# Optimization experiments

Hardware: AMD Instinct MI355X
Metric: run time of the kernel (lower is better)

## Reference

```python
import jax, jax.numpy as jnp
import numpy as np

B, S, D, H = 2, 2048, 1024, 16
HD = D // H  # 64
EPS = 1e-6


def setup_inputs() -> dict:
    key = jax.random.key(0)
    ks = jax.random.split(key, 12)
    s = 1.0 / np.sqrt(D)
    return {
        "query": jax.random.normal(ks[0], (B, S, D), jnp.float32),
        "key": jax.random.normal(ks[1], (B, S, D), jnp.float32),
        "value": jax.random.normal(ks[2], (B, S, D), jnp.float32),
        "mask": jax.random.randint(ks[3], (B, S, S), 0, 2) == 1,
        "Wq": jax.random.normal(ks[4], (D, D), jnp.float32) * s,
        "bq": jnp.zeros((D,), jnp.float32),
        "Wk": jax.random.normal(ks[5], (D, D), jnp.float32) * s,
        "bk": jnp.zeros((D,), jnp.float32),
        "Wv": jax.random.normal(ks[6], (D, D), jnp.float32) * s,
        "bv": jnp.zeros((D,), jnp.float32),
        "Wo": jax.random.normal(ks[7], (D, D), jnp.float32) * s,
        "bo": jnp.zeros((D,), jnp.float32),
        "gamma": jnp.ones((D,), jnp.float32),
        "beta": jnp.zeros((D,), jnp.float32),
    }


def reference(query, key, value, mask, Wq, bq, Wk, bk, Wv, bv, Wo, bo, gamma, beta):
    b, sq, _ = query.shape
    sk = key.shape[1]
    # QKV projections -> [b, h, s, hd]
    q = (query @ Wq + bq).reshape(b, sq, H, HD).transpose(0, 2, 1, 3)
    k = (key @ Wk + bk).reshape(b, sk, H, HD).transpose(0, 2, 1, 3)
    v = (value @ Wv + bv).reshape(b, sk, H, HD).transpose(0, 2, 1, 3)
    # scores [b, h, sq, sk]
    scores = jnp.einsum("bhqd,bhkd->bhqk", q, k) / jnp.sqrt(jnp.float32(HD))
    scores = jnp.where(mask[:, None, :, :], -jnp.inf, scores)
    attn = jax.nn.softmax(scores, axis=-1)  # dropout: eval mode (identity)
    out = jnp.einsum("bhqk,bhkd->bhqd", attn, v)
    out = out.transpose(0, 2, 1, 3).reshape(b, sq, H * HD)
    out = out @ Wo + bo
    # residual + LayerNorm with unbiased std and (std + eps) denominator (faithful to torch code)
    x = query + out
    mean = x.mean(-1, keepdims=True)
    std = jnp.std(x, axis=-1, keepdims=True, ddof=1)
    return gamma * (x - mean) / (std + EPS) + beta
```

## Files before the change

### kernel.cpp

```cpp
#include <hip/hip_runtime.h>


#define NB 2
#define SS 2048
#define DDIM 1024
#define NH 16
#define HDIM 64
#define MROWS (NB * SS)

typedef unsigned short u16;
typedef unsigned long long u64;
typedef unsigned int u32;
typedef short bf16x8 __attribute__((ext_vector_type(8)));
typedef float f32x4 __attribute__((ext_vector_type(4)));

typedef const __attribute__((address_space(1))) void GASV;
typedef __attribute__((address_space(3))) void LASV;

__device__ __forceinline__ float dev_exp2(float x) {
  float r;
  asm("v_exp_f32 %0, %1" : "=v"(r) : "v"(x));
  return r;
}

__device__ __forceinline__ u16 f2bf(float f) {
  unsigned u = __builtin_bit_cast(unsigned, f);
  u += 0x7FFFu + ((u >> 16) & 1u);
  return (u16)(u >> 16);
}

__device__ __forceinline__ u32 cvt_pk_bf16(float a, float b) {
  u32 d;
  asm("v_cvt_pk_bf16_f32 %0, %1, %2" : "=v"(d) : "v"(a), "v"(b));
  return d;
}

__global__ __launch_bounds__(256) void cvt_bf16_3(const float* __restrict__ q,
                                                  const float* __restrict__ k,
                                                  const float* __restrict__ v,
                                                  u16* __restrict__ out) {
  const float* in = (blockIdx.y == 0) ? q : (blockIdx.y == 1) ? k : v;
  size_t i = ((size_t)blockIdx.x * 256 + threadIdx.x) * 4;
  float4 val = *(const float4*)(in + i);
  uint2 o;
  u16* po = (u16*)&o;
  po[0] = f2bf(val.x); po[1] = f2bf(val.y); po[2] = f2bf(val.z); po[3] = f2bf(val.w);
  *(uint2*)(out + (size_t)blockIdx.y * MROWS * DDIM + i) = o;
}

__global__ __launch_bounds__(256) void cvt_mask_bits(const int* __restrict__ in,
                                                     u64* __restrict__ out) {
  size_t w = ((size_t)blockIdx.x * 256 + threadIdx.x) >> 6;
  int lane = threadIdx.x & 63;
  int v = in[w * 64 + lane];
  u64 bits = __ballot(v != 0);
  if (lane == 0) out[w] = bits;
}

__global__ __launch_bounds__(256) void transpose_cvt_w4(const float* __restrict__ W0,
                                                        const float* __restrict__ W1,
                                                        const float* __restrict__ W2,
                                                        const float* __restrict__ W3,
                                                        u16* __restrict__ WTbase) {
  __shared__ u16 t[64][65];
  const int z = blockIdx.z;
  const float* W = (z == 0) ? W0 : (z == 1) ? W1 : (z == 2) ? W2 : W3;
  u16* WT = WTbase + (size_t)z * DDIM * DDIM;
  const int k0 = blockIdx.x * 64, n0 = blockIdx.y * 64;
  const int tid = threadIdx.x;
  const int r = tid >> 4;
  const int c4 = (tid & 15) * 4;
#pragma unroll
  for (int it = 0; it < 4; ++it) {
    int k = r + it * 16;
    float4 v = *(const float4*)&W[(size_t)(k0 + k) * DDIM + n0 + c4];
    t[c4 + 0][k] = f2bf(v.x);
    t[c4 + 1][k] = f2bf(v.y);
    t[c4 + 2][k] = f2bf(v.z);
    t[c4 + 3][k] = f2bf(v.w);
  }
  __syncthreads();
#pragma unroll
  for (int it = 0; it < 4; ++it) {
    int n = r + it * 16;
    uint2 o;
    u16* po = (u16*)&o;
#pragma unroll
    for (int j = 0; j < 4; ++j) po[j] = t[n][c4 + j];
    *(uint2*)&WT[(size_t)(n0 + n) * DDIM + k0 + c4] = o;
  }
}

template <int MODE>
__global__ __launch_bounds__(256) void gemm_bt(const u16* __restrict__ Abase,
                                               const u16* __restrict__ BT,
                                               const float* __restrict__ b0,
                                               const float* __restrict__ b1,
                                               const float* __restrict__ b2,
                                               const float* __restrict__ resid,
                                               void* __restrict__ C,
                                               void* __restrict__ Cv) {
  __shared__ __align__(16) u16 SMEM[2][2][128][64];
  u16(&Al)[2][128][64] = SMEM[0];
  u16(&Bl)[2][128][64] = SMEM[1];
  const int tid = threadIdx.x;
  const int wid = tid >> 6, lane = tid & 63;
  const int wm = (wid >> 1) * 64, wn = (wid & 1) * 64;
  const int NCOL = (MODE == 0) ? 24 : 8;
  const int lin = blockIdx.y * 32 + blockIdx.x;
  const int xcd = lin & 7, idx = lin >> 3;
  const int rowA0 = (xcd * 4 + idx / NCOL) * 128;
  const int colB0 = (idx % NCOL) * 128;
  const int sel = (MODE == 0) ? (colB0 >> 10) : 0;
  const u16* Ag = Abase + (size_t)sel * ((size_t)MROWS * DDIM) + (size_t)rowA0 * DDIM;
  const u16* Bg = BT + (size_t)colB0 * DDIM;
  f32x4 acc[4][4] = {};
  const int rl = lane >> 3;
  const int ce = (lane & 7) * 8;

#define G_STAGE(buf, kt)                                                       \
  do {                                                                         \
    _Pragma("unroll") for (int c = 0; c < 4; ++c) {                            \
      int rt = wid * 32 + c * 8;                                               \
      __builtin_amdgcn_global_load_lds(                                        \
          (GASV*)(Ag + (size_t)(rt + rl) * DDIM + (kt) + ce),                  \
          (LASV*)((char*)&Al[buf][0][0] + rt * 128), 16, 0, 0);                \
      __builtin_amdgcn_global_load_lds(                                        \
          (GASV*)(Bg + (size_t)(rt + rl) * DDIM + (kt) + ce),                  \
          (LASV*)((char*)&Bl[buf][0][0] + rt * 128), 16, 0, 0);                \
    }                                                                          \
  } while (0)

  G_STAGE(0, 0);
  __syncthreads();
  for (int t = 0; t < 16; ++t) {
    const int cur = t & 1;
    if (t < 15) G_STAGE(cur ^ 1, (t + 1) * 64);
#pragma unroll
    for (int kk = 0; kk < 64; kk += 32) {
      bf16x8 af[4], bfr[4];
#pragma unroll
      for (int i = 0; i < 4; ++i)
        af[i] = *(const bf16x8*)&Al[cur][wm + i * 16 + (lane & 15)][kk + (lane >> 4) * 8];
#pragma unroll
      for (int j = 0; j < 4; ++j)
        bfr[j] = *(const bf16x8*)&Bl[cur][wn + j * 16 + (lane & 15)][kk + (lane >> 4) * 8];
#pragma unroll
      for (int i = 0; i < 4; ++i)
#pragma unroll
        for (int j = 0; j < 4; ++j)
          acc[i][j] = __builtin_amdgcn_mfma_f32_16x16x32_bf16(af[i], bfr[j], acc[i][j], 0, 0, 0);
    }
    __syncthreads();
  }
#undef G_STAGE

  const int cb = lane & 15, hi = lane >> 4;
  if (MODE == 0) {
    if (sel == 2) {
      u16(*T)[136] = (u16(*)[136]) & SMEM[0][0][0][0];
      const int dcol0 = colB0 & 1023;
#pragma unroll
      for (int j = 0; j < 4; ++j) {
        int dl = wn + j * 16 + cb;
        float bv = b2[dcol0 + dl];
#pragma unroll
        for (int i = 0; i < 4; ++i) {
          int sl = wm + i * 16 + hi * 4;
          uint2 o;
          o.x = cvt_pk_bf16(acc[i][j][0] + bv, acc[i][j][1] + bv);
          o.y = cvt_pk_bf16(acc[i][j][2] + bv, acc[i][j][3] + bv);
          *(uint2*)&T[dl][sl] = o;
        }
      }
      __syncthreads();
      const int bb = rowA0 >> 11, s0 = rowA0 & (SS - 1);
#pragma unroll
      for (int it = 0; it < 8; ++it) {
        int chunk = it * 256 + tid;
        int dl = chunk >> 4;
        int sc = (chunk & 15) * 8;
        int dg = dcol0 + dl;
        *(bf16x8*)&((u16*)Cv)[((size_t)(bb * NH + (dg >> 6)) * HDIM + (dg & 63)) * SS +
                              s0 + sc] = *(const bf16x8*)&T[dl][sc];
      }
    } else {
      const float* bp = (sel == 0) ? b0 : b1;
      const float scale = (sel == 0) ? 0.125f * 1.44269504088896340736f : 1.0f;
      u16* dst = (u16*)C + (size_t)sel * ((size_t)MROWS * DDIM);
      const int colw0 = (colB0 & 1023) + wn;
#pragma unroll
      for (int i = 0; i < 4; ++i)
#pragma unroll
        for (int j = 0; j < 4; ++j) {
          int colw = colw0 + j * 16 + cb;
          float bv = bp[colw];
#pragma unroll
          for (int r = 0; r < 4; ++r) {
            int row = rowA0 + wm + i * 16 + hi * 4 + r;
            dst[(size_t)row * DDIM + colw] = f2bf((acc[i][j][r] + bv) * scale);
          }
        }
    }
  } else {
#pragma unroll
    for (int i = 0; i < 4; ++i)
#pragma unroll
      for (int j = 0; j < 4; ++j) {
        int col = colB0 + wn + j * 16 + cb;
        float bv = b0[col];
#pragma unroll
        for (int r = 0; r < 4; ++r) {
          int row = rowA0 + wm + i * 16 + hi * 4 + r;
          size_t off = (size_t)row * DDIM + col;
          ((float*)C)[off] = acc[i][j][r] + bv + resid[off];
        }
      }
  }
}

__global__ __launch_bounds__(512, 4) void attn_fwd(const u16* __restrict__ Qp,
                                                   const u16* __restrict__ Kp,
                                                   const u16* __restrict__ VpT,
                                                   const u64* __restrict__ Mbits,
                                                   u16* __restrict__ O) {
  __shared__ __align__(16) u16 Kl[3][64][64];
  __shared__ __align__(16) u16 Vl[3][64][64];
  __shared__ __align__(16) u16 Pl[8][16][64];
  const int tid = threadIdx.x, wid = tid >> 6, lane = tid & 63;
  const int bid = blockIdx.x;
  const int bh = (bid & 7) * 4 + ((bid >> 3) & 3);
  const int q0 = (bid >> 5) * 128;
  const int b = bh >> 4, h = bh & 15;
  const int hi = lane >> 4, cbase = lane & 15, lx = lane & 7;

  bf16x8 qf[2];
  {
    const u16* qb = Qp + (size_t)(b * SS + q0 + wid * 16 + cbase) * DDIM + h * 64 + hi * 8;
    qf[0] = *(const bf16x8*)qb;
    qf[1] = *(const bf16x8*)(qb + 32);
  }
  const bf16x8 ONES8 = {(short)0x3F80, (short)0x3F80, (short)0x3F80, (short)0x3F80,
                        (short)0x3F80, (short)0x3F80, (short)0x3F80, (short)0x3F80};
  f32x4 l_acc = (f32x4){0.f, 0.f, 0.f, 0.f};
  f32x4 accO[4];
#pragma unroll
  for (int f = 0; f < 4; ++f) accO[f] = (f32x4){0.f, 0.f, 0.f, 0.f};

  const u16* Kgb = Kp + (size_t)b * SS * DDIM + h * 64;
  const u16* Vgb = VpT + (size_t)bh * 64 * SS;
  const u64* Mb = Mbits + (size_t)(b * SS + q0 + wid * 16 + cbase) * (SS / 64);
  const int rl = lane >> 3;
  const int ceS = ((lane & 7) ^ rl) * 8;

  int fo[4][2];
#pragma unroll
  for (int f = 0; f < 4; ++f)
#pragma unroll
    for (int ks = 0; ks < 2; ++ks)
      fo[f][ks] = (f * 16 + cbase) * 64 + (((ks * 4 + hi) ^ lx) << 3);
  int pw[4];
#pragma unroll
  for (int f = 0; f < 4; ++f)
    pw[f] = cbase * 64 + (((f * 2 + (hi >> 1)) ^ lx) << 3) + ((hi & 1) << 2);
  u16* KlF = &Kl[0][0][0];
  u16* VlF = &Vl[0][0][0];
  u16* Plw = &Pl[wid][0][0];

#define STAGE_KV(BUF, kv)                                                      \
  do {                                                                         \
    int rt = wid * 8;                                                          \
    __builtin_amdgcn_global_load_lds(                                          \
        (GASV*)(Kgb + (size_t)((kv) + rt + rl) * DDIM + ceS),                  \
        (LASV*)((char*)KlF + (BUF) * 8192 + rt * 128), 16, 0, 0);              \
    __builtin_amdgcn_global_load_lds(                                          \
        (GASV*)(Vgb + (size_t)(rt + rl) * SS + (kv) + ceS),                    \
        (LASV*)((char*)VlF + (BUF) * 8192 + rt * 128), 16, 0, 0);              \
  } while (0)

#define WAITVM(N) asm volatile("s_waitcnt vmcnt(" #N ")" ::: "memory")

#define ATTN_ITER(T, BUF, DO_STAGE, VM)                                        \
  do {                                                                         \
    WAITVM(VM);                                                                \
    __builtin_amdgcn_s_barrier();                                              \
    u64 mrow = Mb[T];                                                          \
    if (DO_STAGE) STAGE_KV(((BUF) + 2) % 3, ((T) + 2) * 64);                   \
    f32x4 sc[4];                                                               \
    __builtin_amdgcn_s_setprio(1);                                             \
    _Pragma("unroll") for (int fn = 0; fn < 4; ++fn) {                         \
      f32x4 c = (f32x4){0.f, 0.f, 0.f, 0.f};                                   \
      _Pragma("unroll") for (int ks = 0; ks < 2; ++ks) {                       \
        bf16x8 kf = *(const bf16x8*)(KlF + (BUF) * 4096 + fo[fn][ks]);         \
        c = __builtin_amdgcn_mfma_f32_16x16x32_bf16(kf, qf[ks], c, 0, 0, 0);   \
      }                                                                        \
      sc[fn] = c;                                                              \
    }                                                                          \
    __builtin_amdgcn_s_setprio(0);                                             \
             \
    u64 mh = mrow >> (hi * 4);                                                 \
    u32 mlo = (u32)mh, mhi2 = (u32)(mh >> 32);                                 \
    _Pragma("unroll") for (int fn = 0; fn < 4; ++fn) {                         \
      u32 b4 = ((fn < 2) ? mlo : mhi2) >> ((fn & 1) * 16);                     \
      _Pragma("unroll") for (int j = 0; j < 4; ++j) {                          \
        float bf_ = (float)((b4 >> j) & 1u);                                   \
        sc[fn][j] = dev_exp2(fmaf(bf_, -512.f, sc[fn][j]));                    \
      }                                                                        \
    }                                                                          \
    _Pragma("unroll") for (int fn = 0; fn < 4; ++fn) {                         \
      uint2 wpair;                                                             \
      wpair.x = cvt_pk_bf16(sc[fn][0], sc[fn][1]);                             \
      wpair.y = cvt_pk_bf16(sc[fn][2], sc[fn][3]);                             \
      *(uint2*)(Plw + pw[fn]) = wpair;                                         \
    }                                                                          \
    bf16x8 pf0 = *(const bf16x8*)(Plw + fo[0][0]);                             \
    bf16x8 pf1 = *(const bf16x8*)(Plw + fo[0][1]);                             \
    __builtin_amdgcn_s_setprio(1);                                             \
    l_acc = __builtin_amdgcn_mfma_f32_16x16x32_bf16(pf0, ONES8, l_acc, 0, 0, 0); \
    l_acc = __builtin_amdgcn_mfma_f32_16x16x32_bf16(pf1, ONES8, l_acc, 0, 0, 0); \
    _Pragma("unroll") for (int nd = 0; nd < 4; ++nd) {                         \
      bf16x8 v0 = *(const bf16x8*)(VlF + (BUF) * 4096 + fo[nd][0]);            \
      bf16x8 v1 = *(const bf16x8*)(VlF + (BUF) * 4096 + fo[nd][1]);            \
      accO[nd] = __builtin_amdgcn_mfma_f32_16x16x32_bf16(pf0, v0, accO[nd], 0, 0, 0); \
      accO[nd] = __builtin_amdgcn_mfma_f32_16x16x32_bf16(pf1, v1, accO[nd], 0, 0, 0); \
    }                                                                          \
    __builtin_amdgcn_s_setprio(0);                                             \
  } while (0)

  STAGE_KV(0, 0);
  STAGE_KV(1, 64);
  for (int t3 = 0; t3 < 30; t3 += 3) {
    ATTN_ITER(t3 + 0, 0, true, 2);
    ATTN_ITER(t3 + 1, 1, true, 2);
    ATTN_ITER(t3 + 2, 2, true, 2);
  }
  ATTN_ITER(30, 0, false, 2);
  ATTN_ITER(31, 1, false, 0);
#undef ATTN_ITER
#undef WAITVM
#undef STAGE_KV

#pragma unroll
  for (int nd = 0; nd < 4; ++nd)
#pragma unroll
    for (int j = 0; j < 4; ++j) {
      int row = q0 + wid * 16 + hi * 4 + j;
      int col = h * 64 + nd * 16 + cbase;
      O[(size_t)(b * SS + row) * DDIM + col] = f2bf(accO[nd][j] / l_acc[j]);
    }
}

__global__ __launch_bounds__(256) void ln_res(const float* __restrict__ xin,
                                              const float* __restrict__ gamma,
                                              const float* __restrict__ beta,
                                              float* __restrict__ out) {
  const int tid = threadIdx.x, wid = tid >> 6, lane = tid & 63;
  const int row = blockIdx.x * 4 + wid;
  const float* xr = xin + (size_t)row * DDIM;
  float4 x[4];
  float s = 0.f;
#pragma unroll
  for (int i = 0; i < 4; ++i) {
    x[i] = *(const float4*)(xr + lane * 4 + i * 256);
    s += (x[i].x + x[i].y) + (x[i].z + x[i].w);
  }
#pragma unroll
  for (int off = 32; off >= 1; off >>= 1) s += __shfl_xor(s, off, 64);
  float mean = s * (1.0f / DDIM);
  float ss = 0.f;
#pragma unroll
  for (int i = 0; i < 4; ++i) {
    x[i].x -= mean; x[i].y -= mean; x[i].z -= mean; x[i].w -= mean;
    ss += (x[i].x * x[i].x + x[i].y * x[i].y) + (x[i].z * x[i].z + x[i].w * x[i].w);
  }
#pragma unroll
  for (int off = 32; off >= 1; off >>= 1) ss += __shfl_xor(ss, off, 64);
  float var = ss * (1.0f / (DDIM - 1));
  float rden = 1.0f / (sqrtf(var) + 1e-6f);
  float* orow = out + (size_t)row * DDIM;
#pragma unroll
  for (int i = 0; i < 4; ++i) {
    float4 g = *(const float4*)(gamma + lane * 4 + i * 256);
    float4 be = *(const float4*)(beta + lane * 4 + i * 256);
    float4 o;
    o.x = g.x * x[i].x * rden + be.x;
    o.y = g.y * x[i].y * rden + be.y;
    o.z = g.z * x[i].z * rden + be.z;
    o.w = g.w * x[i].w * rden + be.w;
    *(float4*)(orow + lane * 4 + i * 256) = o;
  }
}

extern "C" void kernel_launch(void* const* d_in, const int* in_sizes, int n_in,
                              void* d_out, int out_size, void* d_ws, size_t ws_size,
                              hipStream_t stream) {
  const float* query = (const float*)d_in[0];
  const float* key = (const float*)d_in[1];
  const float* value = (const float*)d_in[2];
  const int* mask = (const int*)d_in[3];
  const float* Wq = (const float*)d_in[4];
  const float* bq = (const float*)d_in[5];
  const float* Wk = (const float*)d_in[6];
  const float* bk = (const float*)d_in[7];
  const float* Wv = (const float*)d_in[8];
  const float* bv = (const float*)d_in[9];
  const float* Wo = (const float*)d_in[10];
  const float* bo = (const float*)d_in[11];
  const float* gamma = (const float*)d_in[12];
  const float* beta = (const float*)d_in[13];
  float* out = (float*)d_out;
  char* ws = (char*)d_ws;
  const size_t MB = 1ull << 20;
  u16* qkvb = (u16*)(ws + 0 * MB);
  u16* WT = (u16*)(ws + 24 * MB);
  u16* WoT = (u16*)(ws + 30 * MB);
  u16* Qp = (u16*)(ws + 32 * MB);
  u16* Kp = (u16*)(ws + 40 * MB);
  u16* VpT = (u16*)(ws + 48 * MB);
  u16* attnb = (u16*)(ws + 56 * MB);
  u64* maskbits = (u64*)(ws + 0 * MB);
  float* proj = (float*)(ws + 8 * MB);

  cvt_bf16_3<<<dim3(MROWS * DDIM / 1024, 3), 256, 0, stream>>>(query, key, value, qkvb);
  transpose_cvt_w4<<<dim3(16, 16, 4), 256, 0, stream>>>(Wq, Wk, Wv, Wo, WT);
  gemm_bt<0><<<dim3(32, 24), 256, 0, stream>>>(qkvb, WT, bq, bk, bv, nullptr, Qp, VpT);
  cvt_mask_bits<<<(NB * SS * SS) / 256, 256, 0, stream>>>(mask, maskbits);
  attn_fwd<<<512, 512, 0, stream>>>(Qp, Kp, VpT, maskbits, attnb);
  gemm_bt<1><<<dim3(32, 8), 256, 0, stream>>>(attnb, WoT, bo, nullptr, nullptr,
                                              query, proj, nullptr);
  ln_res<<<MROWS / 4, 256, 0, stream>>>(proj, gamma, beta, out);
}
```

Measured before the change: 153.2 us.

## Fuse fp32-to-bf16 input conversion into QKV GEMM and merge weight/mask prep kernels

The QKV GEMM now loads fp32 query/key/value straight into registers, converts them to bf16 and writes them to LDS, which removes the separate conversion kernel and its 24MB round trip. The weight transpose and mask bit-packing kernels are merged into a single launch. The cost is that the A-tile path no longer uses the async global-to-LDS load. It now needs extra registers and a register-staged write after the MFMA loop, and it reads twice as many bytes per A tile.

New measurement: 171.3 us. 1.12x slower.

```diff
diff --git a/kernel.cpp b/kernel.cpp
--- a/kernel.cpp
+++ b/kernel.cpp
@@ -35,64 +35,55 @@
   return d;
 }
 
-__global__ __launch_bounds__(256) void cvt_bf16_3(const float* __restrict__ q,
-                                                  const float* __restrict__ k,
-                                                  const float* __restrict__ v,
-                                                  u16* __restrict__ out) {
-  const float* in = (blockIdx.y == 0) ? q : (blockIdx.y == 1) ? k : v;
-  size_t i = ((size_t)blockIdx.x * 256 + threadIdx.x) * 4;
-  float4 val = *(const float4*)(in + i);
-  uint2 o;
-  u16* po = (u16*)&o;
-  po[0] = f2bf(val.x); po[1] = f2bf(val.y); po[2] = f2bf(val.z); po[3] = f2bf(val.w);
-  *(uint2*)(out + (size_t)blockIdx.y * MROWS * DDIM + i) = o;
-}
-
-__global__ __launch_bounds__(256) void cvt_mask_bits(const int* __restrict__ in,
-                                                     u64* __restrict__ out) {
-  size_t w = ((size_t)blockIdx.x * 256 + threadIdx.x) >> 6;
-  int lane = threadIdx.x & 63;
-  int v = in[w * 64 + lane];
-  u64 bits = __ballot(v != 0);
-  if (lane == 0) out[w] = bits;
-}
-
-__global__ __launch_bounds__(256) void transpose_cvt_w4(const float* __restrict__ W0,
-                                                        const float* __restrict__ W1,
-                                                        const float* __restrict__ W2,
-                                                        const float* __restrict__ W3,
-                                                        u16* __restrict__ WTbase) {
-  __shared__ u16 t[64][65];
-  const int z = blockIdx.z;
-  const float* W = (z == 0) ? W0 : (z == 1) ? W1 : (z == 2) ? W2 : W3;
-  u16* WT = WTbase + (size_t)z * DDIM * DDIM;
-  const int k0 = blockIdx.x * 64, n0 = blockIdx.y * 64;
-  const int tid = threadIdx.x;
-  const int r = tid >> 4;
-  const int c4 = (tid & 15) * 4;
-#pragma unroll
-  for (int it = 0; it < 4; ++it) {
-    int k = r + it * 16;
-    float4 v = *(const float4*)&W[(size_t)(k0 + k) * DDIM + n0 + c4];
-    t[c4 + 0][k] = f2bf(v.x);
-    t[c4 + 1][k] = f2bf(v.y);
-    t[c4 + 2][k] = f2bf(v.z);
-    t[c4 + 3][k] = f2bf(v.w);
-  }
-  __syncthreads();
-#pragma unroll
-  for (int it = 0; it < 4; ++it) {
-    int n = r + it * 16;
-    uint2 o;
-    u16* po = (u16*)&o;
-#pragma unroll
-    for (int j = 0; j < 4; ++j) po[j] = t[n][c4 + j];
-    *(uint2*)&WT[(size_t)(n0 + n) * DDIM + k0 + c4] = o;
+__global__ __launch_bounds__(256) void prep_wm(const float* __restrict__ W0,
+                                               const float* __restrict__ W1,
+                                               const float* __restrict__ W2,
+                                               const float* __restrict__ W3,
+                                               u16* __restrict__ WTbase,
+                                               const int* __restrict__ maskin,
+                                               u64* __restrict__ mbits) {
+  const int bid = blockIdx.x, tid = threadIdx.x;
+  if (bid < 1024) {
+    __shared__ u16 t[64][65];
+    const int z = bid >> 8;
+    const float* W = (z == 0) ? W0 : (z == 1) ? W1 : (z == 2) ? W2 : W3;
+    u16* WT = WTbase + (size_t)z * DDIM * DDIM;
+    const int k0 = ((bid >> 4) & 15) * 64, n0 = (bid & 15) * 64;
+    const int r = tid >> 4;
+    const int c4 = (tid & 15) * 4;
+#pragma unroll
+    for (int it = 0; it < 4; ++it) {
+      int k = r + it * 16;
+      float4 v = *(const float4*)&W[(size_t)(k0 + k) * DDIM + n0 + c4];
+      t[c4 + 0][k] = f2bf(v.x);
+      t[c4 + 1][k] = f2bf(v.y);
+      t[c4 + 2][k] = f2bf(v.z);
+      t[c4 + 3][k] = f2bf(v.w);
+    }
+    __syncthreads();
+#pragma unroll
+    for (int it = 0; it < 4; ++it) {
+      int n = r + it * 16;
+      uint2 o;
+      u16* po = (u16*)&o;
+#pragma unroll
+      for (int j = 0; j < 4; ++j) po[j] = t[n][c4 + j];
+      *(uint2*)&WT[(size_t)(n0 + n) * DDIM + k0 + c4] = o;
+    }
+  } else {
+    size_t w = ((size_t)(bid - 1024) * 256 + tid) >> 6;
+    int lane = tid & 63;
+    int v = maskin[w * 64 + lane];
+    u64 bits = __ballot(v != 0);
+    if (lane == 0) mbits[w] = bits;
   }
 }
 
 template <int MODE>
-__global__ __launch_bounds__(256) void gemm_bt(const u16* __restrict__ Abase,
+__global__ __launch_bounds__(256) void gemm_bt(const float* __restrict__ Af0,
+                                               const float* __restrict__ Af1,
+                                               const float* __restrict__ Af2,
+                                               const u16* __restrict__ Abf,
                                                const u16* __restrict__ BT,
                                                const float* __restrict__ b0,
                                                const float* __restrict__ b1,
@@ -112,30 +103,79 @@
   const int rowA0 = (xcd * 4 + idx / NCOL) * 128;
   const int colB0 = (idx % NCOL) * 128;
   const int sel = (MODE == 0) ? (colB0 >> 10) : 0;
-  const u16* Ag = Abase + (size_t)sel * ((size_t)MROWS * DDIM) + (size_t)rowA0 * DDIM;
+  const float* Af = nullptr;
+  const u16* Ag = nullptr;
+  if (MODE == 0) {
+    Af = ((sel == 0) ? Af0 : (sel == 1) ? Af1 : Af2) + (size_t)rowA0 * DDIM;
+  } else {
+    Ag = Abf + (size_t)rowA0 * DDIM;
+  }
   const u16* Bg = BT + (size_t)colB0 * DDIM;
   f32x4 acc[4][4] = {};
   const int rl = lane >> 3;
   const int ce = (lane & 7) * 8;
 
-#define G_STAGE(buf, kt)                                                       \
+  float4 pa0[4], pa1[4];
+
+#define A_LOADF(kt)                                                            \
+  do {                                                                         \
+    _Pragma("unroll") for (int c = 0; c < 4; ++c) {                            \
+      int row = wid * 32 + c * 8 + rl;                                         \
+      pa0[c] = *(const float4*)(Af + (size_t)row * DDIM + (kt) + ce);          \
+      pa1[c] = *(const float4*)(Af + (size_t)row * DDIM + (kt) + ce + 4);      \
+    }                                                                          \
+  } while (0)
+
+#define A_WRITEF(buf)                                                          \
+  do {                                                                         \
+    _Pragma("unroll") for (int c = 0; c < 4; ++c) {                            \
+      int row = wid * 32 + c * 8 + rl;                                         \
+      bf16x8 w;                                                                \
+      u32* pw32 = (u32*)&w;                                                    \
+      pw32[0] = cvt_pk_bf16(pa0[c].x, pa0[c].y);                               \
+      pw32[1] = cvt_pk_bf16(pa0[c].z, pa0[c].w);                               \
+      pw32[2] = cvt_pk_bf16(pa1[c].x, pa1[c].y);                               \
+      pw32[3] = cvt_pk_bf16(pa1[c].z, pa1[c].w);                               \
+      *(bf16x8*)&Al[buf][row][ce] = w;                                         \
+    }                                                                          \
+  } while (0)
+
+#define A_GLOAD(buf, kt)                                                       \
   do {                                                                         \
     _Pragma("unroll") for (int c = 0; c < 4; ++c) {                            \
       int rt = wid * 32 + c * 8;                                               \
       __builtin_amdgcn_global_load_lds(                                        \
           (GASV*)(Ag + (size_t)(rt + rl) * DDIM + (kt) + ce),                  \
           (LASV*)((char*)&Al[buf][0][0] + rt * 128), 16, 0, 0);                \
+    }                                                                          \
+  } while (0)
+
+#define B_STAGE(buf, kt)                                                       \
+  do {                                                                         \
+    _Pragma("unroll") for (int c = 0; c < 4; ++c) {                            \
+      int rt = wid * 32 + c * 8;                                               \
       __builtin_amdgcn_global_load_lds(                                        \
           (GASV*)(Bg + (size_t)(rt + rl) * DDIM + (kt) + ce),                  \
           (LASV*)((char*)&Bl[buf][0][0] + rt * 128), 16, 0, 0);                \
     }                                                                          \
   } while (0)
 
-  G_STAGE(0, 0);
+  if (MODE == 0) {
+    A_LOADF(0);
+    B_STAGE(0, 0);
+    A_WRITEF(0);
+  } else {
+    A_GLOAD(0, 0);
+    B_STAGE(0, 0);
+  }
   __syncthreads();
   for (int t = 0; t < 16; ++t) {
     const int cur = t & 1;
-    if (t < 15) G_STAGE(cur ^ 1, (t + 1) * 64);
+    if (t < 15) {
+      if (MODE == 0) A_LOADF((t + 1) * 64);
+      else A_GLOAD(cur ^ 1, (t + 1) * 64);
+      B_STAGE(cur ^ 1, (t + 1) * 64);
+    }
 #pragma unroll
     for (int kk = 0; kk < 64; kk += 32) {
       bf16x8 af[4], bfr[4];
@@ -151,9 +191,13 @@
         for (int j = 0; j < 4; ++j)
           acc[i][j] = __builtin_amdgcn_mfma_f32_16x16x32_bf16(af[i], bfr[j], acc[i][j], 0, 0, 0);
     }
+    if (MODE == 0 && t < 15) A_WRITEF(cur ^ 1);
     __syncthreads();
   }
-#undef G_STAGE
+#undef A_LOADF
+#undef A_WRITEF
+#undef A_GLOAD
+#undef B_STAGE
 
   const int cb = lane & 15, hi = lane >> 4;
   if (MODE == 0) {
@@ -411,22 +455,22 @@
   float* out = (float*)d_out;
   char* ws = (char*)d_ws;
   const size_t MB = 1ull << 20;
-  u16* qkvb = (u16*)(ws + 0 * MB);
+  u64* maskbits = (u64*)(ws + 0 * MB);
+  float* proj = (float*)(ws + 8 * MB);
   u16* WT = (u16*)(ws + 24 * MB);
   u16* WoT = (u16*)(ws + 30 * MB);
   u16* Qp = (u16*)(ws + 32 * MB);
   u16* Kp = (u16*)(ws + 40 * MB);
   u16* VpT = (u16*)(ws + 48 * MB);
   u16* attnb = (u16*)(ws + 56 * MB);
-  u64* maskbits = (u64*)(ws + 0 * MB);
-  float* proj = (float*)(ws + 8 * MB);
-
-  cvt_bf16_3<<<dim3(MROWS * DDIM / 1024, 3), 256, 0, stream>>>(query, key, value, qkvb);
-  transpose_cvt_w4<<<dim3(16, 16, 4), 256, 0, stream>>>(Wq, Wk, Wv, Wo, WT);
-  gemm_bt<0><<<dim3(32, 24), 256, 0, stream>>>(qkvb, WT, bq, bk, bv, nullptr, Qp, VpT);
-  cvt_mask_bits<<<(NB * SS * SS) / 256, 256, 0, stream>>>(mask, maskbits);
+
+  prep_wm<<<1024 + (NB * SS * SS) / 256, 256, 0, stream>>>(Wq, Wk, Wv, Wo, WT,
+                                                           mask, maskbits);
+  gemm_bt<0><<<dim3(32, 24), 256, 0, stream>>>(query, key, value, nullptr, WT,
+                                               bq, bk, bv, nullptr, Qp, VpT);
   attn_fwd<<<512, 512, 0, stream>>>(Qp, Kp, VpT, maskbits, attnb);
-  gemm_bt<1><<<dim3(32, 8), 256, 0, stream>>>(attnb, WoT, bo, nullptr, nullptr,
-                                              query, proj, nullptr);
+  gemm_bt<1><<<dim3(32, 8), 256, 0, stream>>>(nullptr, nullptr, nullptr, attnb,
+                                              WoT, bo, nullptr, nullptr, query,
+                                              proj, nullptr);
   ln_res<<<MROWS / 4, 256, 0, stream>>>(proj, gamma, beta, out);
 }
```
